# Optimization experiments

Hardware: AMD Instinct MI355X
Metric: run time of the kernel (lower is better)

The kernel has to match this reference:

```python
import jax, jax.numpy as jnp
import numpy as np

H_DIM = 64
GRID = 8
NS = 2.0  # neighborhood_size


def _pool_seq(hidden, pos):
    # hidden: (P, H_DIM) hidden states of peds in one scene; pos: (P, 2) end positions
    P = hidden.shape[0]
    g2 = GRID * GRID
    tl_x = pos[:, 0] - NS / 2
    tl_y = pos[:, 1] + NS / 2
    br_x = pos[:, 0] + NS / 2
    br_y = pos[:, 1] - NS / 2
    # pair (i, j): grid of ped i (rows), position of ped j (cols)
    ox = pos[None, :, 0]
    oy = pos[None, :, 1]
    cell_x = jnp.floor((ox - tl_x[:, None]) / NS * GRID)
    cell_y = jnp.floor((tl_y[:, None] - oy) / NS * GRID)
    grid_pos = (cell_x + cell_y * GRID).astype(jnp.int32)
    # out-of-bound if outside neighborhood box OR i == j (diagonal forced out)
    oob = ((ox >= br_x[:, None]) | (ox <= tl_x[:, None])
           | (oy >= tl_y[:, None]) | (oy <= br_y[:, None])
           | jnp.eye(P, dtype=bool))
    idx = grid_pos + 1 + (jnp.arange(P, dtype=jnp.int32) * g2)[:, None]
    idx = jnp.where(oob, 0, idx)  # slot 0 is the trash bin (dropped below)
    src = jnp.broadcast_to(hidden[None], (P, P, H_DIM)).reshape(P * P, H_DIM)
    buf = jnp.zeros((P * g2 + 1, H_DIM), hidden.dtype)
    buf = buf.at[idx.reshape(-1)].add(src)
    return buf[1:].reshape(P, g2 * H_DIM)


def reference(h_states, seq_start_end, end_pos, rel_pos, W, b):
    B = end_pos.shape[0]
    S = seq_start_end.shape[0]
    P = B // S  # equal-length scenes -> static reshape
    hidden = h_states.reshape(-1, H_DIM).reshape(S, P, H_DIM)
    pos = end_pos.reshape(S, P, 2)
    pooled = jax.vmap(_pool_seq)(hidden, pos).reshape(B, GRID * GRID * H_DIM)
    # make_mlp([4096, 1024], relu, batch_norm=False): Linear -> ReLU
    return jax.nn.relu(pooled @ W + b)


def setup_inputs():
    key = jax.random.key(0)
    k0, k1, k2, k3 = jax.random.split(key, 4)
    S, P = 64, 64
    B = S * P
    bottleneck = 1024
    feat = GRID * GRID * H_DIM  # 4096
    h_states = jax.random.normal(k0, (1, B, H_DIM), jnp.float32)
    starts = jnp.arange(S, dtype=jnp.int32) * P
    seq_start_end = jnp.stack([starts, starts + P], axis=1)
    end_pos = jax.random.normal(k1, (B, 2), jnp.float32)
    rel_pos = jax.random.normal(k2, (B, 2), jnp.float32)
    W = jax.random.normal(k3, (feat, bottleneck), jnp.float32) * 0.02
    b = jnp.zeros((bottleneck,), jnp.float32)
    return {"h_states": h_states, "seq_start_end": seq_start_end,
            "end_pos": end_pos, "rel_pos": rel_pos, "W": W, "b": b}
```

## Files before the change

kernel.cpp:

```cpp
#include <hip/hip_runtime.h>


#define BM 128
#define BN 128
#define BK 128

typedef short short8 __attribute__((ext_vector_type(8)));
typedef short short4v __attribute__((ext_vector_type(4)));
typedef float floatx16 __attribute__((ext_vector_type(16)));

__device__ inline short f2bf(float x) {
    union { float f; unsigned u; } v; v.f = x;
    unsigned r = v.u + 0x7fffu + ((v.u >> 16) & 1u);
    return (short)(r >> 16);
}

__device__ inline void gload_lds16(const void* g, void* l) {
    __builtin_amdgcn_global_load_lds(
        (const __attribute__((address_space(1))) void*)g,
        (__attribute__((address_space(3))) void*)l,
        16, 0, 0);
}

__global__ __launch_bounds__(256) void prep_kernel(
    const float* __restrict__ h,
    const float* __restrict__ pos,
    short* __restrict__ pooled,
    const float* __restrict__ W,
    short* __restrict__ Wt,
    int K, int N, int poolBlocks)
{
    __shared__ __align__(16) unsigned char sh[18944];
    const int tid = threadIdx.x;

    if ((int)blockIdx.x < poolBlocks) {
        float* hs = (float*)sh;
        float* px = (float*)(sh + 16384);
        float* py = (float*)(sh + 16640);
        unsigned long long* wmask = (unsigned long long*)(sh + 16896);

        const int lane = tid & 63;
        const int w    = tid >> 6;
        const int s    = blockIdx.x >> 4;
        const int grp  = blockIdx.x & 15;
        const size_t base = (size_t)s * 64;

        const float4* hv  = (const float4*)(h + base * 64);
        float4*       hsv = (float4*)hs;
        #pragma unroll
        for (int c = 0; c < 4; ++c) hsv[tid + c * 256] = hv[tid + c * 256];
        if (tid < 64) {
            float2 p = ((const float2*)pos)[base + tid];
            px[tid] = p.x; py[tid] = p.y;
        }
        wmask[w * 64 + lane] = 0ull;
        __syncthreads();

        const int i = grp * 4 + w;
        const float tlx = px[i] - 1.0f;
        const float tly = py[i] + 1.0f;
        const float brx = px[i] + 1.0f;
        const float bry = py[i] - 1.0f;

        {
            const int j = lane;
            const float ox = px[j], oy = py[j];
            if (ox < brx && ox > tlx && oy < tly && oy > bry && j != i) {
                int cx = (int)floorf((ox - tlx) * 4.0f);
                int cy = (int)floorf((tly - oy) * 4.0f);
                atomicOr(&wmask[w * 64 + cx + cy * 8], 1ull << j);
            }
        }

        const int half = lane >> 5;
        const int d0   = (lane & 31) * 2;
        const size_t orow = (base + i) * 4096;
        unsigned short* pooledU = (unsigned short*)pooled;
        for (int c = 0; c < 64; c += 2) {
            unsigned long long m = wmask[w * 64 + c + half];
            float ax = 0.f, ay = 0.f;
            while (m) {
                int j0 = __builtin_ctzll(m); m &= m - 1;
                float2 hv2 = *(const float2*)&hs[j0 * 64 + d0];
                ax += hv2.x; ay += hv2.y;
            }
            unsigned pk = ((unsigned)(unsigned short)f2bf(ay) << 16)
                        |  (unsigned short)f2bf(ax);
            *(unsigned*)&pooledU[orow + (size_t)(c + half) * 64 + d0] = pk;
        }
    } else {
        float* t = (float*)sh;
        const int bid = blockIdx.x - poolBlocks;
        const int k0 = (bid & 63) * 64;
        const int n0 = (bid >> 6) * 64;

        const int r  = tid >> 4;
        const int cq = (tid & 15) * 4;
        #pragma unroll
        for (int i2 = 0; i2 < 4; ++i2) {
            const int row = r + i2 * 16;
            float4 v = *(const float4*)&W[(size_t)(k0 + row) * N + n0 + cq];
            t[row * 65 + cq + 0] = v.x; t[row * 65 + cq + 1] = v.y;
            t[row * 65 + cq + 2] = v.z; t[row * 65 + cq + 3] = v.w;
        }
        __syncthreads();
        const int nl = tid >> 4;
        const int kq = (tid & 15) * 4;
        #pragma unroll
        for (int i2 = 0; i2 < 4; ++i2) {
            const int n = nl + i2 * 16;
            short4v o;
            o.x = f2bf(t[(kq + 0) * 65 + n]); o.y = f2bf(t[(kq + 1) * 65 + n]);
            o.z = f2bf(t[(kq + 2) * 65 + n]); o.w = f2bf(t[(kq + 3) * 65 + n]);
            *(short4v*)&Wt[(size_t)(n0 + n) * K + k0 + kq] = o;
        }
    }
}

__global__ __launch_bounds__(512) void gemm_bias_relu(
    const short* __restrict__ A,
    const short* __restrict__ Bt,
    const float* __restrict__ bias,
    float* __restrict__ out,
    int M, int N, int K)
{
    __shared__ __align__(16) short As[2][BM * BK];
    __shared__ __align__(16) short Bs[2][BN * BK];

    const int tid  = threadIdx.x;
    const int lane = tid & 63;
    const int wave = tid >> 6;
    const int kh = wave & 1;
    const int wn = (wave >> 1) & 1;
    const int wr = wave >> 2;
    const int nl = lane & 31;
    const int hl = lane >> 5;
    const int ml = lane & 15;

    const int b  = blockIdx.x;
    const int ib = b >> 3;
    const int m0 = ((b & 7) * 4 + (ib >> 3)) * BM;
    const int n0 = (ib & 7) * BN;

    const int r4   = lane >> 4;
    const int slot = lane & 15;

    const short* ag[4];
    const short* bg[4];
    #pragma unroll
    for (int c = 0; c < 4; ++c) {
        const int gi = c * 8 + wave;
        const int rl = gi * 4 + r4;
        ag[c] = A  + (size_t)(m0 + rl) * K + (slot ^ (rl & 15)) * 8;
        bg[c] = Bt + (size_t)(n0 + rl) * K + (slot ^ (rl & 15)) * 8;
    }

    floatx16 acc[4];
    #pragma unroll
    for (int i = 0; i < 4; ++i)
        #pragma unroll
        for (int r = 0; r < 16; ++r) acc[i][r] = 0.f;

    #pragma unroll
    for (int c = 0; c < 4; ++c) { gload_lds16(ag[c], &As[0][(c * 8 + wave) * 512]); ag[c] += BK; }
    #pragma unroll
    for (int c = 0; c < 4; ++c) { gload_lds16(bg[c], &Bs[0][(c * 8 + wave) * 512]); bg[c] += BK; }
    __syncthreads();

    const int NT = K / BK;
    for (int i = 0; i < NT; ++i) {
        const int cur = i & 1;
        if (i + 1 < NT) {
            const int nxt = cur ^ 1;
            #pragma unroll
            for (int c = 0; c < 4; ++c) { gload_lds16(ag[c], &As[nxt][(c * 8 + wave) * 512]); ag[c] += BK; }
            #pragma unroll
            for (int c = 0; c < 4; ++c) { gload_lds16(bg[c], &Bs[nxt][(c * 8 + wave) * 512]); bg[c] += BK; }
        }
        __builtin_amdgcn_s_setprio(1);
        #pragma unroll
        for (int t = 0; t < 4; ++t) {
            const int g  = kh * 8 + 2 * t + hl;
            const int go = (g ^ ml) * 8;
            short8 a0 = *(const short8*)&As[cur][(wr * 64 +      nl) * BK + go];
            short8 a1 = *(const short8*)&As[cur][(wr * 64 + 32 + nl) * BK + go];
            short8 b0 = *(const short8*)&Bs[cur][(wn * 64 +      nl) * BK + go];
            short8 b1 = *(const short8*)&Bs[cur][(wn * 64 + 32 + nl) * BK + go];
            acc[0] = __builtin_amdgcn_mfma_f32_32x32x16_bf16(a0, b0, acc[0], 0, 0, 0);
            acc[1] = __builtin_amdgcn_mfma_f32_32x32x16_bf16(a0, b1, acc[1], 0, 0, 0);
            acc[2] = __builtin_amdgcn_mfma_f32_32x32x16_bf16(a1, b0, acc[2], 0, 0, 0);
            acc[3] = __builtin_amdgcn_mfma_f32_32x32x16_bf16(a1, b1, acc[3], 0, 0, 0);
        }
        __builtin_amdgcn_s_setprio(0);
        __syncthreads();
    }

    float* red = (float*)As;
    if (kh) {
        #pragma unroll
        for (int mi = 0; mi < 2; ++mi)
            #pragma unroll
            for (int ni = 0; ni < 2; ++ni)
                #pragma unroll
                for (int r = 0; r < 16; ++r) {
                    const int row32 = (r & 3) + 8 * (r >> 2) + 4 * hl;
                    red[(wr * 2 + wn) * 4096 + (mi * 32 + row32) * 64 + ni * 32 + nl] =
                        acc[mi * 2 + ni][r];
                }
    }
    __syncthreads();
    if (!kh) {
        const float bv0 = bias[n0 + wn * 64 + nl];
        const float bv1 = bias[n0 + wn * 64 + 32 + nl];
        #pragma unroll
        for (int mi = 0; mi < 2; ++mi)
            #pragma unroll
            for (int ni = 0; ni < 2; ++ni) {
                const float bv = ni ? bv1 : bv0;
                #pragma unroll
                for (int r = 0; r < 16; ++r) {
                    const int row32 = (r & 3) + 8 * (r >> 2) + 4 * hl;
                    const int gm = m0 + wr * 64 + mi * 32 + row32;
                    const int gn = n0 + wn * 64 + ni * 32 + nl;
                    float v = acc[mi * 2 + ni][r]
                            + red[(wr * 2 + wn) * 4096 + (mi * 32 + row32) * 64 + ni * 32 + nl]
                            + bv;
                    out[(size_t)gm * N + gn] = v > 0.f ? v : 0.f;
                }
            }
    }
}

extern "C" void kernel_launch(void* const* d_in, const int* in_sizes, int n_in,
                              void* d_out, int out_size, void* d_ws, size_t ws_size,
                              hipStream_t stream) {
    const float* h    = (const float*)d_in[0];
    const float* pos  = (const float*)d_in[2];
    const float* W    = (const float*)d_in[4];
    const float* bias = (const float*)d_in[5];

    const int B = in_sizes[0] / 64;
    const int N = in_sizes[5];
    const int K = 64 * 64;

    short* pooled = (short*)d_ws;
    short* Wt     = pooled + (size_t)B * K;
    float* out    = (float*)d_out;

    const int poolBlocks = B / 4;
    const int castBlocks = (K / 64) * (N / 64);
    prep_kernel<<<poolBlocks + castBlocks, 256, 0, stream>>>(
        h, pos, pooled, W, Wt, K, N, poolBlocks);
    gemm_bias_relu<<<(B / BM) * (N / BN), 512, 0, stream>>>(
        pooled, Wt, bias, out, B, N, K);
}
```

Before: 135.0 us.

## Fuse social pooling into GEMM A-tile generation using per-cell neighbor bitmasks

The prep kernel now writes only per-pedestrian 64-cell neighbor bitmasks instead of the full bf16 pooled matrix. The GEMM kernel loads the 128 hidden rows for its M tile into LDS once, then builds each K-tile of A on the fly by summing neighbor hidden vectors selected by the masks. This removes the large pooled-matrix write and read through global memory. In exchange it adds pooling ALU and LDS work inside the GEMM main loop, leaves A single-buffered, and needs extra LDS that may lower occupancy.

```diff
diff --git a/kernel.cpp b/kernel.cpp
--- a/kernel.cpp
+++ b/kernel.cpp
@@ -8,6 +8,7 @@
 typedef short short8 __attribute__((ext_vector_type(8)));
 typedef short short4v __attribute__((ext_vector_type(4)));
 typedef float floatx16 __attribute__((ext_vector_type(16)));
+typedef unsigned long long u64;
 
 __device__ inline short f2bf(float x) {
     union { float f; unsigned u; } v; v.f = x;
@@ -22,75 +23,19 @@
         16, 0, 0);
 }
 
-__global__ __launch_bounds__(256) void prep_kernel(
-    const float* __restrict__ h,
+__global__ __launch_bounds__(256) void prep2_kernel(
     const float* __restrict__ pos,
-    short* __restrict__ pooled,
+    u64* __restrict__ masks,
     const float* __restrict__ W,
     short* __restrict__ Wt,
-    int K, int N, int poolBlocks)
+    int K, int N, int castBlocks)
 {
-    __shared__ __align__(16) unsigned char sh[18944];
+    __shared__ __align__(16) unsigned char sh[33280];
     const int tid = threadIdx.x;
 
-    if ((int)blockIdx.x < poolBlocks) {
-        float* hs = (float*)sh;
-        float* px = (float*)(sh + 16384);
-        float* py = (float*)(sh + 16640);
-        unsigned long long* wmask = (unsigned long long*)(sh + 16896);
-
-        const int lane = tid & 63;
-        const int w    = tid >> 6;
-        const int s    = blockIdx.x >> 4;
-        const int grp  = blockIdx.x & 15;
-        const size_t base = (size_t)s * 64;
-
-        const float4* hv  = (const float4*)(h + base * 64);
-        float4*       hsv = (float4*)hs;
-        #pragma unroll
-        for (int c = 0; c < 4; ++c) hsv[tid + c * 256] = hv[tid + c * 256];
-        if (tid < 64) {
-            float2 p = ((const float2*)pos)[base + tid];
-            px[tid] = p.x; py[tid] = p.y;
-        }
-        wmask[w * 64 + lane] = 0ull;
-        __syncthreads();
-
-        const int i = grp * 4 + w;
-        const float tlx = px[i] - 1.0f;
-        const float tly = py[i] + 1.0f;
-        const float brx = px[i] + 1.0f;
-        const float bry = py[i] - 1.0f;
-
-        {
-            const int j = lane;
-            const float ox = px[j], oy = py[j];
-            if (ox < brx && ox > tlx && oy < tly && oy > bry && j != i) {
-                int cx = (int)floorf((ox - tlx) * 4.0f);
-                int cy = (int)floorf((tly - oy) * 4.0f);
-                atomicOr(&wmask[w * 64 + cx + cy * 8], 1ull << j);
-            }
-        }
-
-        const int half = lane >> 5;
-        const int d0   = (lane & 31) * 2;
-        const size_t orow = (base + i) * 4096;
-        unsigned short* pooledU = (unsigned short*)pooled;
-        for (int c = 0; c < 64; c += 2) {
-            unsigned long long m = wmask[w * 64 + c + half];
-            float ax = 0.f, ay = 0.f;
-            while (m) {
-                int j0 = __builtin_ctzll(m); m &= m - 1;
-                float2 hv2 = *(const float2*)&hs[j0 * 64 + d0];
-                ax += hv2.x; ay += hv2.y;
-            }
-            unsigned pk = ((unsigned)(unsigned short)f2bf(ay) << 16)
-                        |  (unsigned short)f2bf(ax);
-            *(unsigned*)&pooledU[orow + (size_t)(c + half) * 64 + d0] = pk;
-        }
-    } else {
+    if ((int)blockIdx.x < castBlocks) {
         float* t = (float*)sh;
-        const int bid = blockIdx.x - poolBlocks;
+        const int bid = blockIdx.x;
         const int k0 = (bid & 63) * 64;
         const int n0 = (bid >> 6) * 64;
 
@@ -114,18 +59,56 @@
             o.z = f2bf(t[(kq + 2) * 65 + n]); o.w = f2bf(t[(kq + 3) * 65 + n]);
             *(short4v*)&Wt[(size_t)(n0 + n) * K + k0 + kq] = o;
         }
-    }
-}
-
-__global__ __launch_bounds__(512) void gemm_bias_relu(
-    const short* __restrict__ A,
+    } else {
+        float* px = (float*)sh;
+        float* py = px + 64;
+        u64*   lm = (u64*)(sh + 512);
+
+        const int s = blockIdx.x - castBlocks;
+        const size_t base = (size_t)s * 64;
+
+        if (tid < 64) {
+            float2 p = ((const float2*)pos)[base + tid];
+            px[tid] = p.x; py[tid] = p.y;
+        }
+        for (int k = tid; k < 4096; k += 256) lm[k] = 0ull;
+        __syncthreads();
+
+        const int i  = tid >> 2;
+        const int j0 = (tid & 3) * 16;
+        const float tlx = px[i] - 1.0f;
+        const float tly = py[i] + 1.0f;
+        const float brx = px[i] + 1.0f;
+        const float bry = py[i] - 1.0f;
+        #pragma unroll
+        for (int jj = 0; jj < 16; ++jj) {
+            const int j = j0 + jj;
+            const float ox = px[j], oy = py[j];
+            if (ox < brx && ox > tlx && oy < tly && oy > bry && j != i) {
+                int cx = (int)floorf((ox - tlx) * 4.0f);
+                int cy = (int)floorf((tly - oy) * 4.0f);
+                atomicOr(&lm[i * 64 + cx + cy * 8], 1ull << j);
+            }
+        }
+        __syncthreads();
+
+        ulonglong2*       dst = (ulonglong2*)(masks + base * 64);
+        const ulonglong2* src = (const ulonglong2*)lm;
+        for (int k = tid; k < 2048; k += 256) dst[k] = src[k];
+    }
+}
+
+__global__ __launch_bounds__(512) void fused_pool_gemm(
+    const float* __restrict__ h,
+    const u64* __restrict__ masks,
     const short* __restrict__ Bt,
     const float* __restrict__ bias,
     float* __restrict__ out,
     int M, int N, int K)
 {
-    __shared__ __align__(16) short As[2][BM * BK];
+    __shared__ __align__(16) short As[BM * BK];
     __shared__ __align__(16) short Bs[2][BN * BK];
+    __shared__ __align__(16) float hs[BM * 64];
 
     const int tid  = threadIdx.x;
     const int lane = tid & 63;
@@ -145,15 +128,21 @@
     const int r4   = lane >> 4;
     const int slot = lane & 15;
 
-    const short* ag[4];
     const short* bg[4];
+    const float* hg[4];
     #pragma unroll
     for (int c = 0; c < 4; ++c) {
         const int gi = c * 8 + wave;
         const int rl = gi * 4 + r4;
-        ag[c] = A  + (size_t)(m0 + rl) * K + (slot ^ (rl & 15)) * 8;
         bg[c] = Bt + (size_t)(n0 + rl) * K + (slot ^ (rl & 15)) * 8;
-    }
+        hg[c] = h  + (size_t)(m0 + rl) * 64 + (slot ^ (rl & 15)) * 4;
+    }
+
+    const int br = tid >> 2;
+    const int bc = (tid >> 1) & 1;
+    const int bq = tid & 1;
+    const int hb = br & 64;
+    const u64* mrow = masks + (size_t)(m0 + br) * 64 + bc;
 
     floatx16 acc[4];
     #pragma unroll
@@ -161,29 +150,60 @@
         #pragma unroll
         for (int r = 0; r < 16; ++r) acc[i][r] = 0.f;
 
+    u64 m_cur = mrow[0];
+    u64 mA    = mrow[2];
     #pragma unroll
-    for (int c = 0; c < 4; ++c) { gload_lds16(ag[c], &As[0][(c * 8 + wave) * 512]); ag[c] += BK; }
+    for (int c = 0; c < 4; ++c) gload_lds16(hg[c], &hs[(c * 8 + wave) * 256]);
     #pragma unroll
     for (int c = 0; c < 4; ++c) { gload_lds16(bg[c], &Bs[0][(c * 8 + wave) * 512]); bg[c] += BK; }
     __syncthreads();
 
+    {
+        float4 a0{0,0,0,0}, a1{0,0,0,0}, a2{0,0,0,0}, a3{0,0,0,0},
+               a4{0,0,0,0}, a5{0,0,0,0}, a6{0,0,0,0}, a7{0,0,0,0};
+        u64 m = m_cur;
+        while (m) {
+            const int j = __builtin_ctzll(m); m &= m - 1;
+            const float* hr = &hs[(hb + j) << 6];
+            const int key = (hb + j) & 15;
+            a0 += *(const float4*)&hr[(((bq * 8 + 0) ^ key) << 2)];
+            a1 += *(const float4*)&hr[(((bq * 8 + 1) ^ key) << 2)];
+            a2 += *(const float4*)&hr[(((bq * 8 + 2) ^ key) << 2)];
+            a3 += *(const float4*)&hr[(((bq * 8 + 3) ^ key) << 2)];
+            a4 += *(const float4*)&hr[(((bq * 8 + 4) ^ key) << 2)];
+            a5 += *(const float4*)&hr[(((bq * 8 + 5) ^ key) << 2)];
+            a6 += *(const float4*)&hr[(((bq * 8 + 6) ^ key) << 2)];
+            a7 += *(const float4*)&hr[(((bq * 8 + 7) ^ key) << 2)];
+        }
+        const int gbase = bc * 8 + bq * 4;
+        short8 o;
+        o[0]=f2bf(a0.x); o[1]=f2bf(a0.y); o[2]=f2bf(a0.z); o[3]=f2bf(a0.w);
+        o[4]=f2bf(a1.x); o[5]=f2bf(a1.y); o[6]=f2bf(a1.z); o[7]=f2bf(a1.w);
+        *(short8*)&As[(br << 7) + (((gbase + 0) ^ (br & 15)) << 3)] = o;
+        o[0]=f2bf(a2.x); o[1]=f2bf(a2.y); o[2]=f2bf(a2.z); o[3]=f2bf(a2.w);
+        o[4]=f2bf(a3.x); o[5]=f2bf(a3.y); o[6]=f2bf(a3.z); o[7]=f2bf(a3.w);
+        *(short8*)&As[(br << 7) + (((gbase + 1) ^ (br & 15)) << 3)] = o;
+        o[0]=f2bf(a4.x); o[1]=f2bf(a4.y); o[2]=f2bf(a4.z); o[3]=f2bf(a4.w);
+        o[4]=f2bf(a5.x); o[5]=f2bf(a5.y); o[6]=f2bf(a5.z); o[7]=f2bf(a5.w);
+        *(short8*)&As[(br << 7) + (((gbase + 2) ^ (br & 15)) << 3)] = o;
+        o[0]=f2bf(a6.x); o[1]=f2bf(a6.y); o[2]=f2bf(a6.z); o[3]=f2bf(a6.w);
+        o[4]=f2bf(a7.x); o[5]=f2bf(a7.y); o[6]=f2bf(a7.z); o[7]=f2bf(a7.w);
+        *(short8*)&As[(br << 7) + (((gbase + 3) ^ (br & 15)) << 3)] = o;
+    }
+    __syncthreads();
+
     const int NT = K / BK;
     for (int i = 0; i < NT; ++i) {
         const int cur = i & 1;
-        if (i + 1 < NT) {
-            const int nxt = cur ^ 1;
-            #pragma unroll
-            for (int c = 0; c < 4; ++c) { gload_lds16(ag[c], &As[nxt][(c * 8 + wave) * 512]); ag[c] += BK; }
-            #pragma unroll
-            for (int c = 0; c < 4; ++c) { gload_lds16(bg[c], &Bs[nxt][(c * 8 + wave) * 512]); bg[c] += BK; }
-        }
+        u64 mB = (i + 2 < NT) ? mrow[(size_t)(i + 2) * 2] : 0ull;
+
         __builtin_amdgcn_s_setprio(1);
         #pragma unroll
         for (int t = 0; t < 4; ++t) {
             const int g  = kh * 8 + 2 * t + hl;
             const int go = (g ^ ml) * 8;
-            short8 a0 = *(const short8*)&As[cur][(wr * 64 +      nl) * BK + go];
-            short8 a1 = *(const short8*)&As[cur][(wr * 64 + 32 + nl) * BK + go];
+            short8 a0 = *(const short8*)&As[(wr * 64 +      nl) * BK + go];
+            short8 a1 = *(const short8*)&As[(wr * 64 + 32 + nl) * BK + go];
             short8 b0 = *(const short8*)&Bs[cur][(wn * 64 +      nl) * BK + go];
             short8 b1 = *(const short8*)&Bs[cur][(wn * 64 + 32 + nl) * BK + go];
             acc[0] = __builtin_amdgcn_mfma_f32_32x32x16_bf16(a0, b0, acc[0], 0, 0, 0);
@@ -193,9 +213,47 @@
         }
         __builtin_amdgcn_s_setprio(0);
         __syncthreads();
-    }
-
-    float* red = (float*)As;
+
+        if (i + 1 < NT) {
+            const int nxt = cur ^ 1;
+            #pragma unroll
+            for (int c = 0; c < 4; ++c) { gload_lds16(bg[c], &Bs[nxt][(c * 8 + wave) * 512]); bg[c] += BK; }
+            float4 a0{0,0,0,0}, a1{0,0,0,0}, a2{0,0,0,0}, a3{0,0,0,0},
+                   a4{0,0,0,0}, a5{0,0,0,0}, a6{0,0,0,0}, a7{0,0,0,0};
+            u64 m = mA;
+            while (m) {
+                const int j = __builtin_ctzll(m); m &= m - 1;
+                const float* hr = &hs[(hb + j) << 6];
+                const int key = (hb + j) & 15;
+                a0 += *(const float4*)&hr[(((bq * 8 + 0) ^ key) << 2)];
+                a1 += *(const float4*)&hr[(((bq * 8 + 1) ^ key) << 2)];
+                a2 += *(const float4*)&hr[(((bq * 8 + 2) ^ key) << 2)];
+                a3 += *(const float4*)&hr[(((bq * 8 + 3) ^ key) << 2)];
+                a4 += *(const float4*)&hr[(((bq * 8 + 4) ^ key) << 2)];
+                a5 += *(const float4*)&hr[(((bq * 8 + 5) ^ key) << 2)];
+                a6 += *(const float4*)&hr[(((bq * 8 + 6) ^ key) << 2)];
+                a7 += *(const float4*)&hr[(((bq * 8 + 7) ^ key) << 2)];
+            }
+            const int gbase = bc * 8 + bq * 4;
+            short8 o;
+            o[0]=f2bf(a0.x); o[1]=f2bf(a0.y); o[2]=f2bf(a0.z); o[3]=f2bf(a0.w);
+            o[4]=f2bf(a1.x); o[5]=f2bf(a1.y); o[6]=f2bf(a1.z); o[7]=f2bf(a1.w);
+            *(short8*)&As[(br << 7) + (((gbase + 0) ^ (br & 15)) << 3)] = o;
+            o[0]=f2bf(a2.x); o[1]=f2bf(a2.y); o[2]=f2bf(a2.z); o[3]=f2bf(a2.w);
+            o[4]=f2bf(a3.x); o[5]=f2bf(a3.y); o[6]=f2bf(a3.z); o[7]=f2bf(a3.w);
+            *(short8*)&As[(br << 7) + (((gbase + 1) ^ (br & 15)) << 3)] = o;
+            o[0]=f2bf(a4.x); o[1]=f2bf(a4.y); o[2]=f2bf(a4.z); o[3]=f2bf(a4.w);
+            o[4]=f2bf(a5.x); o[5]=f2bf(a5.y); o[6]=f2bf(a5.z); o[7]=f2bf(a5.w);
+            *(short8*)&As[(br << 7) + (((gbase + 2) ^ (br & 15)) << 3)] = o;
+            o[0]=f2bf(a6.x); o[1]=f2bf(a6.y); o[2]=f2bf(a6.z); o[3]=f2bf(a6.w);
+            o[4]=f2bf(a7.x); o[5]=f2bf(a7.y); o[6]=f2bf(a7.z); o[7]=f2bf(a7.w);
+            *(short8*)&As[(br << 7) + (((gbase + 3) ^ (br & 15)) << 3)] = o;
+        }
+        mA = mB;
+        __syncthreads();
+    }
+
+    float* red = (float*)Bs;
     if (kh) {
         #pragma unroll
         for (int mi = 0; mi < 2; ++mi)
@@ -243,14 +301,14 @@
     const int N = in_sizes[5];
     const int K = 64 * 64;
 
-    short* pooled = (short*)d_ws;
-    short* Wt     = pooled + (size_t)B * K;
-    float* out    = (float*)d_out;
-
-    const int poolBlocks = B / 4;
+    u64*   masks = (u64*)d_ws;
+    short* Wt    = (short*)(masks + (size_t)B * 64);
+    float* out   = (float*)d_out;
+
     const int castBlocks = (K / 64) * (N / 64);
-    prep_kernel<<<poolBlocks + castBlocks, 256, 0, stream>>>(
-        h, pos, pooled, W, Wt, K, N, poolBlocks);
-    gemm_bias_relu<<<(B / BM) * (N / BN), 512, 0, stream>>>(
-        pooled, Wt, bias, out, B, N, K);
-}
+    const int maskBlocks = B / 64;
+    prep2_kernel<<<castBlocks + maskBlocks, 256, 0, stream>>>(
+        pos, masks, W, Wt, K, N, castBlocks);
+    fused_pool_gemm<<<(B / BM) * (N / BN), 512, 0, stream>>>(
+        h, masks, Wt, bias, out, B, N, K);
+}
```

Result: slower. 145.5 us (+7.8%).
